# Kernel tuning notes

Hardware: AMD Instinct MI355X
Metric: run time of the kernel (lower is better)

Reference implementation:

```python
import jax, jax.numpy as jnp
import numpy as np

B, T, D = 2, 2048, 1024
H = 16
DH = D // H


def setup_inputs() -> dict:
    key = jax.random.key(0)
    ks = jax.random.split(key, 6)
    s = 1.0 / np.sqrt(D)
    return {
        "x": jax.random.normal(ks[0], (B, T, D), dtype=jnp.float32),
        "Wq": jax.random.normal(ks[1], (D, D), dtype=jnp.float32) * s,
        "Wk": jax.random.normal(ks[2], (D, D), dtype=jnp.float32) * s,
        "Wv": jax.random.normal(ks[3], (D, D), dtype=jnp.float32) * s,
        "Wo": jax.random.normal(ks[4], (D, D), dtype=jnp.float32) * s,
        "bo": jax.random.normal(ks[5], (D,), dtype=jnp.float32) * s,
    }


def reference(x, Wq, Wk, Wv, Wo, bo):
    b, t, _ = x.shape
    # separate Q/K/V projections (nn.Linear: x @ W.T, no bias)
    q = (x @ Wq.T).reshape(b, t, H, DH).transpose(0, 2, 1, 3)  # [b,h,t,hd]
    k = (x @ Wk.T).reshape(b, t, H, DH).transpose(0, 2, 1, 3)
    v = (x @ Wv.T).reshape(b, t, H, DH).transpose(0, 2, 1, 3)

    scores = jnp.einsum("bhqd,bhkd->bhqk", q, k)  # [b,h,t,t]
    causal = jnp.triu(jnp.ones((t, t), dtype=bool), k=1)
    scores = jnp.where(causal, -jnp.inf, scores)
    weights = jax.nn.softmax(scores / np.sqrt(DH), axis=-1)
    # dropout p=0.0 -> identity
    ctx = jnp.einsum("bhqk,bhkd->bhqd", weights, v)  # [b,h,t,hd]
    # NOTE: original code reshapes WITHOUT transposing heads back — replicate faithfully
    ctx = ctx.reshape(b, t, H * DH)
    return ctx @ Wo.T + bo
```

## Files before the change

### kernel.cpp

```cpp
#include <hip/hip_runtime.h>
#include <math.h>

#define BATCH 2
#define SEQ   2048
#define DIM   1024
#define NH    16
#define HD    64
#define MTOT  4096

typedef __attribute__((ext_vector_type(8)))  short bf16x8;
typedef __attribute__((ext_vector_type(4)))  float f32x4;
typedef __attribute__((ext_vector_type(16))) float f32x16;

__device__ __forceinline__ ushort f2bf(float f) {
    union { float f; unsigned u; } v; v.f = f;
    unsigned r = v.u + 0x7fffu + ((v.u >> 16) & 1u);
    return (ushort)(r >> 16);
}

__device__ __forceinline__ unsigned cvtpk_bf16(float lo, float hi) {
    unsigned r;
    asm("v_cvt_pk_bf16_f32 %0, %1, %2" : "=v"(r) : "v"(lo), "v"(hi));
    return r;
}

__global__ __launch_bounds__(256)
void cast_all(const float* __restrict__ x,
              const float* __restrict__ Wq, const float* __restrict__ Wk,
              const float* __restrict__ Wv, const float* __restrict__ Wo,
              ushort* __restrict__ xb,
              ushort* __restrict__ wqb, ushort* __restrict__ wkb,
              ushort* __restrict__ wvb, ushort* __restrict__ wob)
{
    const int z = blockIdx.y;
    const float* s; ushort* d; int n4;
    if (z == 0)      { s = x;  d = xb;  n4 = MTOT * DIM / 4; }
    else if (z == 1) { s = Wq; d = wqb; n4 = DIM * DIM / 4; }
    else if (z == 2) { s = Wk; d = wkb; n4 = DIM * DIM / 4; }
    else if (z == 3) { s = Wv; d = wvb; n4 = DIM * DIM / 4; }
    else             { s = Wo; d = wob; n4 = DIM * DIM / 4; }
    for (int i = blockIdx.x * blockDim.x + threadIdx.x; i < n4;
         i += gridDim.x * blockDim.x) {
        float4 v = ((const float4*)s)[i];
        ushort4 o;
        o.x = f2bf(v.x); o.y = f2bf(v.y); o.z = f2bf(v.z); o.w = f2bf(v.w);
        ((ushort4*)d)[i] = o;
    }
}

template<int MODE>
__global__ __launch_bounds__(256)
void gemm_bf16(const ushort* __restrict__ A,
               const ushort* __restrict__ W0, const ushort* __restrict__ W1,
               const ushort* __restrict__ W2,
               ushort* __restrict__ D0, ushort* __restrict__ D1,
               ushort* __restrict__ D2,
               const float* __restrict__ bias, float* __restrict__ Fout)
{
    __shared__ __align__(16) ushort As[2][128 * 64];
    __shared__ __align__(16) ushort Bs[2][128 * 64];

    const int tid = threadIdx.x;
    const int w = tid >> 6, l = tid & 63;
    const int g = l >> 4, l15 = l & 15;
    const int wr = w >> 1, wc = w & 1;
    const int brow = blockIdx.x * 128, bcol = blockIdx.y * 128;

    const ushort* W = (MODE == 1) ? W0
                    : (blockIdx.z == 0 ? W0 : (blockIdx.z == 1 ? W1 : W2));
    ushort* Dst = (MODE == 1) ? (ushort*)0
                : (blockIdx.z == 0 ? D0 : (blockIdx.z == 1 ? D1 : D2));

    const int rsub = l >> 3;
    const int gc   = ((l & 7) ^ rsub) * 8;
    const size_t arow0 = (size_t)(brow + 32 * w + rsub) * DIM;
    const size_t brow0 = (size_t)(bcol + 32 * w + rsub) * DIM;

    auto STAGE = [&](int buf, int ktel) {
        #pragma unroll
        for (int i = 0; i < 4; ++i) {
            __builtin_amdgcn_global_load_lds(
                (const __attribute__((address_space(1))) void*)
                    &A[arow0 + (size_t)(8 * i) * DIM + ktel + gc],
                (__attribute__((address_space(3))) void*)
                    &As[buf][(32 * w + 8 * i) * 64], 16, 0, 0);
            __builtin_amdgcn_global_load_lds(
                (const __attribute__((address_space(1))) void*)
                    &W[brow0 + (size_t)(8 * i) * DIM + ktel + gc],
                (__attribute__((address_space(3))) void*)
                    &Bs[buf][(32 * w + 8 * i) * 64], 16, 0, 0);
        }
    };

    STAGE(0, 0);
    STAGE(1, 64);

    f32x4 acc[4][4] = {};

    for (int t = 0; t < 16; ++t) {
        const int cur = t & 1;
        if (t < 15) asm volatile("s_waitcnt vmcnt(8)" ::: "memory");
        else        asm volatile("s_waitcnt vmcnt(0)" ::: "memory");
        __builtin_amdgcn_s_barrier();
        __builtin_amdgcn_sched_barrier(0);

        #pragma unroll
        for (int kh = 0; kh < 2; ++kh) {
            bf16x8 af[4], bfr[4];
            #pragma unroll
            for (int mi = 0; mi < 4; ++mi) {
                int row = 64 * wr + 16 * mi + l15;
                af[mi] = *(const bf16x8*)&As[cur][row * 64 + (((4 * kh + g) ^ (row & 7)) * 8)];
            }
            #pragma unroll
            for (int nj = 0; nj < 4; ++nj) {
                int row = 64 * wc + 16 * nj + l15;
                bfr[nj] = *(const bf16x8*)&Bs[cur][row * 64 + (((4 * kh + g) ^ (row & 7)) * 8)];
            }
            __builtin_amdgcn_s_setprio(1);
            #pragma unroll
            for (int mi = 0; mi < 4; ++mi)
                #pragma unroll
                for (int nj = 0; nj < 4; ++nj)
                    acc[mi][nj] = __builtin_amdgcn_mfma_f32_16x16x32_bf16(
                        af[mi], bfr[nj], acc[mi][nj], 0, 0, 0);
            __builtin_amdgcn_s_setprio(0);
        }

        __builtin_amdgcn_sched_barrier(0);
        __builtin_amdgcn_s_barrier();
        if (t + 2 < 16) STAGE(cur, (t + 2) * 64);
    }

    if (MODE == 0) {
        const float osc = (blockIdx.z == 0) ? 0.125f : 1.0f;
        if (blockIdx.z == 2) {
            #pragma unroll
            for (int mi = 0; mi < 4; ++mi)
                #pragma unroll
                for (int nj = 0; nj < 4; ++nj)
                    #pragma unroll
                    for (int reg = 0; reg < 4; ++reg) {
                        int row = brow + 64 * wr + 16 * mi + 4 * g + reg;
                        int col = bcol + 64 * wc + 16 * nj + l15;
                        int b = row >> 11, t = row & (SEQ - 1);
                        int hh = col >> 6, hd = col & 63;
                        Dst[(size_t)(b * NH + hh) * SEQ * HD
                            + ((size_t)(t >> 3) * 64 + hd) * 8 + (t & 7)] =
                            f2bf(acc[mi][nj][reg]);
                    }
        } else {
            #pragma unroll
            for (int mi = 0; mi < 4; ++mi)
                #pragma unroll
                for (int nj = 0; nj < 4; ++nj)
                    #pragma unroll
                    for (int reg = 0; reg < 4; ++reg) {
                        int row = brow + 64 * wr + 16 * mi + 4 * g + reg;
                        int col = bcol + 64 * wc + 16 * nj + l15;
                        int b = row >> 11, t = row & (SEQ - 1);
                        int hh = col >> 6, hd = col & 63;
                        Dst[(size_t)(b * NH + hh) * SEQ * HD
                            + (((size_t)(t >> 5) * 8 + (hd >> 3)) * 32 + (t & 31)) * 8
                            + (hd & 7)] = f2bf(acc[mi][nj][reg] * osc);
                    }
        }
    } else {
        #pragma unroll
        for (int nj = 0; nj < 4; ++nj) {
            int col = bcol + 64 * wc + 16 * nj + l15;
            float bv = bias[col];
            #pragma unroll
            for (int mi = 0; mi < 4; ++mi)
                #pragma unroll
                for (int reg = 0; reg < 4; ++reg) {
                    int row = brow + 64 * wr + 16 * mi + 4 * g + reg;
                    Fout[(size_t)row * DIM + col] = acc[mi][nj][reg] + bv;
                }
        }
    }
}

__global__ __launch_bounds__(64, 2)
void attn_mfma5(const ushort* __restrict__ q, const ushort* __restrict__ k,
                const ushort* __restrict__ vt, ushort* __restrict__ ctx)
{
    __shared__ __align__(16) ushort Ob[32 * 64];

    const int l = threadIdx.x;
    const int l31 = l & 31, h = l >> 5;
    const int bh = blockIdx.x;
    const int qt = 63 - (int)blockIdx.y;
    const int qlo = qt * 32;
    const int last = qt >> 1;
    const float LOG2E = 1.44269504f;

    const ushort* Qg = q  + (size_t)bh * SEQ * HD;
    const ushort* Kg = k  + (size_t)bh * SEQ * HD;
    const ushort* Vg = vt + (size_t)bh * SEQ * HD;

    bf16x8 qf[4];
    #pragma unroll
    for (int s = 0; s < 4; ++s)
        qf[s] = *(const bf16x8*)&Qg[(((size_t)qt * 8 + 2 * s + h) * 32 + l31) * 8];

    f32x16 o[2] = {};
    float m = -3.0e38f, lsum = 0.f;

    bf16x8 kfA[8], kfB[8], vfA[8], vfB[8];
    #pragma unroll
    for (int s = 0; s < 4; ++s)
        #pragma unroll
        for (int f = 0; f < 2; ++f)
            kfA[2 * s + f] = *(const bf16x8*)
                &Kg[(((size_t)f * 8 + 2 * s + h) * 32 + l31) * 8];
    #pragma unroll
    for (int s4 = 0; s4 < 4; ++s4)
        #pragma unroll
        for (int dt = 0; dt < 2; ++dt)
            vfA[2 * s4 + dt] = *(const bf16x8*)
                &Vg[(((size_t)(2 * s4 + h)) * 64 + 32 * dt + l31) * 8];

    auto body = [&](bf16x8 (&kc)[8], bf16x8 (&kn)[8],
                    bf16x8 (&vc)[8], bf16x8 (&vn)[8], int kt) {
        const int kvb = 64 * kt;

        f32x16 st[2] = {};
        #pragma unroll
        for (int s = 0; s < 4; ++s)
            #pragma unroll
            for (int f = 0; f < 2; ++f)
                st[f] = __builtin_amdgcn_mfma_f32_32x32x16_bf16(
                    kc[2 * s + f], qf[s], st[f], 0, 0, 0);

        if (kt < last) {
            #pragma unroll
            for (int s = 0; s < 4; ++s)
                #pragma unroll
                for (int f = 0; f < 2; ++f)
                    kn[2 * s + f] = *(const bf16x8*)
                        &Kg[(((size_t)(2 * kt + 2 + f) * 8 + 2 * s + h) * 32 + l31) * 8];
            #pragma unroll
            for (int s4 = 0; s4 < 4; ++s4)
                #pragma unroll
                for (int dt = 0; dt < 2; ++dt)
                    vn[2 * s4 + dt] = *(const bf16x8*)
                        &Vg[(((size_t)(8 * kt + 8 + 2 * s4 + h)) * 64 + 32 * dt + l31) * 8];
        }

        const int qg = qlo + l31;
        if (kvb + 63 > qlo) {
            #pragma unroll
            for (int f = 0; f < 2; ++f)
                #pragma unroll
                for (int r = 0; r < 16; ++r) {
                    int kvg = kvb + 32 * f + (r & 3) + 8 * (r >> 2) + 4 * h;
                    if (kvg > qg) st[f][r] = -INFINITY;
                }
        }

        float mx[8];
        #pragma unroll
        for (int i2 = 0; i2 < 8; ++i2) {
            const int f = i2 >> 2, rb = 4 * (i2 & 3);
            mx[i2] = fmaxf(fmaxf(st[f][rb], st[f][rb + 1]),
                           fmaxf(st[f][rb + 2], st[f][rb + 3]));
        }
        float tmax = fmaxf(fmaxf(fmaxf(mx[0], mx[1]), fmaxf(mx[2], mx[3])),
                           fmaxf(fmaxf(mx[4], mx[5]), fmaxf(mx[6], mx[7])));
        tmax = fmaxf(tmax, __shfl_xor(tmax, 32));
        float ty = fmaxf(tmax * LOG2E, -3.0e38f);

        if (!__all(ty - m <= 8.0f)) {
            float mn = fmaxf(m, ty);
            float sc = exp2f(m - mn);
            lsum *= sc;
            #pragma unroll
            for (int dt = 0; dt < 2; ++dt)
                #pragma unroll
                for (int r = 0; r < 16; ++r) o[dt][r] *= sc;
            m = mn;
        }

        float ls0 = 0.f, ls1 = 0.f, ls2 = 0.f, ls3 = 0.f;
        #pragma unroll
        for (int f = 0; f < 2; ++f)
            #pragma unroll
            for (int r = 0; r < 16; ++r) {
                float pv = exp2f(fmaf(st[f][r], LOG2E, -m));
                st[f][r] = pv;
                if ((r & 3) == 0) ls0 += pv;
                else if ((r & 3) == 1) ls1 += pv;
                else if ((r & 3) == 2) ls2 += pv;
                else ls3 += pv;
            }
        lsum += (ls0 + ls1) + (ls2 + ls3);

        #pragma unroll
        for (int s4 = 0; s4 < 4; ++s4) {
            const int f = s4 >> 1, rb2 = 8 * (s4 & 1);
            unsigned Aa = cvtpk_bf16(st[f][rb2 + 0], st[f][rb2 + 1]);
            unsigned Bb = cvtpk_bf16(st[f][rb2 + 2], st[f][rb2 + 3]);
            unsigned Cc = cvtpk_bf16(st[f][rb2 + 4], st[f][rb2 + 5]);
            unsigned Dd = cvtpk_bf16(st[f][rb2 + 6], st[f][rb2 + 7]);
            unsigned Ax = (unsigned)__shfl_xor((int)Aa, 32);
            unsigned Bx = (unsigned)__shfl_xor((int)Bb, 32);
            unsigned Cx = (unsigned)__shfl_xor((int)Cc, 32);
            unsigned Dx = (unsigned)__shfl_xor((int)Dd, 32);
            union { unsigned wv[4]; bf16x8 v; } pu;
            pu.wv[0] = h ? Cx : Aa;
            pu.wv[1] = h ? Dx : Bb;
            pu.wv[2] = h ? Cc : Ax;
            pu.wv[3] = h ? Dd : Bx;
            #pragma unroll
            for (int dt = 0; dt < 2; ++dt)
                o[dt] = __builtin_amdgcn_mfma_f32_32x32x16_bf16(
                    vc[2 * s4 + dt], pu.v, o[dt], 0, 0, 0);
        }
    };

    int kt = 0;
    while (true) {
        body(kfA, kfB, vfA, vfB, kt);
        if (++kt > last) break;
        body(kfB, kfA, vfB, vfA, kt);
        if (++kt > last) break;
    }

    float lt = lsum + __shfl_xor(lsum, 32);
    float inv = 1.0f / lt;

    #pragma unroll
    for (int dt = 0; dt < 2; ++dt)
        #pragma unroll
        for (int r = 0; r < 16; r += 2) {
            int d = 32 * dt + (r & 3) + 8 * (r >> 2) + 4 * h;
            unsigned wrd = cvtpk_bf16(o[dt][r] * inv, o[dt][r + 1] * inv);
            *(unsigned*)&Ob[l31 * 64 + (((d >> 3) ^ (l31 & 7)) * 8) + (d & 7)] = wrd;
        }
    asm volatile("s_waitcnt lgkmcnt(0)" ::: "memory");
    __builtin_amdgcn_sched_barrier(0);

    ushort* Cg = ctx + (size_t)bh * SEQ * HD + (size_t)qlo * HD;
    #pragma unroll
    for (int i = 0; i < 4; ++i) {
        int qq = l >> 1, c = (l & 1) * 4 + i;
        int4 vvv = *(const int4*)&Ob[qq * 64 + ((c ^ (qq & 7)) * 8)];
        *(int4*)&Cg[qq * 64 + c * 8] = vvv;
    }
}

extern "C" void kernel_launch(void* const* d_in, const int* in_sizes, int n_in,
                              void* d_out, int out_size, void* d_ws, size_t ws_size,
                              hipStream_t stream)
{
    (void)in_sizes; (void)n_in; (void)out_size; (void)ws_size;
    const float* x  = (const float*)d_in[0];
    const float* Wq = (const float*)d_in[1];
    const float* Wk = (const float*)d_in[2];
    const float* Wv = (const float*)d_in[3];
    const float* Wo = (const float*)d_in[4];
    const float* bo = (const float*)d_in[5];
    float* out = (float*)d_out;

    ushort* wsu  = (ushort*)d_ws;
    ushort* xb   = wsu;
    ushort* wqb  = wsu + 4194304;
    ushort* wkb  = wsu + 5242880;
    ushort* wvb  = wsu + 6291456;
    ushort* wob  = wsu + 7340032;
    ushort* qbuf = wsu + 8388608;
    ushort* kbuf = wsu + 12582912;
    ushort* vtb  = wsu + 16777216;
    ushort* ctxb = wsu + 20971520;

    cast_all<<<dim3(512, 5), 256, 0, stream>>>(x, Wq, Wk, Wv, Wo,
                                               xb, wqb, wkb, wvb, wob);

    dim3 gqkv(MTOT / 128, DIM / 128, 3);
    gemm_bf16<0><<<gqkv, 256, 0, stream>>>(xb, wqb, wkb, wvb,
                                           qbuf, kbuf, vtb, nullptr, nullptr);

    dim3 ga(BATCH * NH, SEQ / 32);
    attn_mfma5<<<ga, 64, 0, stream>>>(qbuf, kbuf, vtb, ctxb);

    dim3 go(MTOT / 128, DIM / 128, 1);
    gemm_bf16<1><<<go, 256, 0, stream>>>(ctxb, wob, nullptr, nullptr,
                                         nullptr, nullptr, nullptr, bo, out);
}
```

Before: 116.3 us.

## Split attention KV range across four waves and merge partial softmax in LDS

The attention kernel now launches 256 threads per block, and each of the four waves processes a contiguous quarter of the causal KV tiles for the same 32-query tile. Each wave keeps its own online-softmax state. The partial max, sum and output values are then combined through LDS with a rescale-and-add reduction before the bf16 context is written. This split-K style parallelism shortens the serial KV loop per block and should help the long late query tiles. The cost is extra LDS traffic (32KB of fp32 partials), two block barriers, and idle waves on short early tiles.

Measured after the change: 244.9 us. 110% more time.

```diff
diff --git a/kernel.cpp b/kernel.cpp
--- a/kernel.cpp
+++ b/kernel.cpp
@@ -181,18 +181,24 @@
     }
 }
 
-__global__ __launch_bounds__(64, 2)
-void attn_mfma5(const ushort* __restrict__ q, const ushort* __restrict__ k,
+__global__ __launch_bounds__(256, 4)
+void attn_mfma6(const ushort* __restrict__ q, const ushort* __restrict__ k,
                 const ushort* __restrict__ vt, ushort* __restrict__ ctx)
 {
-    __shared__ __align__(16) ushort Ob[32 * 64];
-
-    const int l = threadIdx.x;
+    __shared__ float Olds[4 * 2048];
+    __shared__ float Mlds[4][32];
+    __shared__ float Llds[4][32];
+
+    const int tid = threadIdx.x;
+    const int wq = tid >> 6, l = tid & 63;
     const int l31 = l & 31, h = l >> 5;
     const int bh = blockIdx.x;
     const int qt = 63 - (int)blockIdx.y;
     const int qlo = qt * 32;
-    const int last = qt >> 1;
+    const int nt  = (qt >> 1) + 1;
+    const int cnt = (nt + 3) >> 2;
+    const int kt0 = wq * cnt;
+    const int kt1 = min(nt, kt0 + cnt);
     const float LOG2E = 1.44269504f;
 
     const ushort* Qg = q  + (size_t)bh * SEQ * HD;
@@ -207,147 +213,160 @@
     f32x16 o[2] = {};
     float m = -3.0e38f, lsum = 0.f;
 
-    bf16x8 kfA[8], kfB[8], vfA[8], vfB[8];
-    #pragma unroll
-    for (int s = 0; s < 4; ++s)
-        #pragma unroll
-        for (int f = 0; f < 2; ++f)
-            kfA[2 * s + f] = *(const bf16x8*)
-                &Kg[(((size_t)f * 8 + 2 * s + h) * 32 + l31) * 8];
-    #pragma unroll
-    for (int s4 = 0; s4 < 4; ++s4)
-        #pragma unroll
-        for (int dt = 0; dt < 2; ++dt)
-            vfA[2 * s4 + dt] = *(const bf16x8*)
-                &Vg[(((size_t)(2 * s4 + h)) * 64 + 32 * dt + l31) * 8];
-
-    auto body = [&](bf16x8 (&kc)[8], bf16x8 (&kn)[8],
-                    bf16x8 (&vc)[8], bf16x8 (&vn)[8], int kt) {
-        const int kvb = 64 * kt;
-
-        f32x16 st[2] = {};
+    if (kt0 < kt1) {
+        bf16x8 kfA[8], kfB[8], vfA[8], vfB[8];
         #pragma unroll
         for (int s = 0; s < 4; ++s)
             #pragma unroll
             for (int f = 0; f < 2; ++f)
-                st[f] = __builtin_amdgcn_mfma_f32_32x32x16_bf16(
-                    kc[2 * s + f], qf[s], st[f], 0, 0, 0);
-
-        if (kt < last) {
+                kfA[2 * s + f] = *(const bf16x8*)
+                    &Kg[(((size_t)(2 * kt0 + f) * 8 + 2 * s + h) * 32 + l31) * 8];
+        #pragma unroll
+        for (int s4 = 0; s4 < 4; ++s4)
+            #pragma unroll
+            for (int dt = 0; dt < 2; ++dt)
+                vfA[2 * s4 + dt] = *(const bf16x8*)
+                    &Vg[(((size_t)(8 * kt0 + 2 * s4 + h)) * 64 + 32 * dt + l31) * 8];
+
+        auto body = [&](bf16x8 (&kc)[8], bf16x8 (&kn)[8],
+                        bf16x8 (&vc)[8], bf16x8 (&vn)[8], int kt) {
+            const int kvb = 64 * kt;
+
+            f32x16 st[2] = {};
             #pragma unroll
             for (int s = 0; s < 4; ++s)
                 #pragma unroll
                 for (int f = 0; f < 2; ++f)
-                    kn[2 * s + f] = *(const bf16x8*)
-                        &Kg[(((size_t)(2 * kt + 2 + f) * 8 + 2 * s + h) * 32 + l31) * 8];
-            #pragma unroll
-            for (int s4 = 0; s4 < 4; ++s4)
+                    st[f] = __builtin_amdgcn_mfma_f32_32x32x16_bf16(
+                        kc[2 * s + f], qf[s], st[f], 0, 0, 0);
+
+            if (kt + 1 < kt1) {
+                #pragma unroll
+                for (int s = 0; s < 4; ++s)
+                    #pragma unroll
+                    for (int f = 0; f < 2; ++f)
+                        kn[2 * s + f] = *(const bf16x8*)
+                            &Kg[(((size_t)(2 * kt + 2 + f) * 8 + 2 * s + h) * 32 + l31) * 8];
+                #pragma unroll
+                for (int s4 = 0; s4 < 4; ++s4)
+                    #pragma unroll
+                    for (int dt = 0; dt < 2; ++dt)
+                        vn[2 * s4 + dt] = *(const bf16x8*)
+                            &Vg[(((size_t)(8 * kt + 8 + 2 * s4 + h)) * 64 + 32 * dt + l31) * 8];
+            }
+
+            const int qg = qlo + l31;
+            if (kvb + 63 > qlo) {
+                #pragma unroll
+                for (int f = 0; f < 2; ++f)
+                    #pragma unroll
+                    for (int r = 0; r < 16; ++r) {
+                        int kvg = kvb + 32 * f + (r & 3) + 8 * (r >> 2) + 4 * h;
+                        if (kvg > qg) st[f][r] = -INFINITY;
+                    }
+            }
+
+            float mx[8];
+            #pragma unroll
+            for (int i2 = 0; i2 < 8; ++i2) {
+                const int f = i2 >> 2, rb = 4 * (i2 & 3);
+                mx[i2] = fmaxf(fmaxf(st[f][rb], st[f][rb + 1]),
+                               fmaxf(st[f][rb + 2], st[f][rb + 3]));
+            }
+            float tmax = fmaxf(fmaxf(fmaxf(mx[0], mx[1]), fmaxf(mx[2], mx[3])),
+                               fmaxf(fmaxf(mx[4], mx[5]), fmaxf(mx[6], mx[7])));
+            tmax = fmaxf(tmax, __shfl_xor(tmax, 32));
+            float ty = fmaxf(tmax * LOG2E, -3.0e38f);
+
+            if (!__all(ty - m <= 8.0f)) {
+                float mn = fmaxf(m, ty);
+                float sc = exp2f(m - mn);
+                lsum *= sc;
                 #pragma unroll
                 for (int dt = 0; dt < 2; ++dt)
-                    vn[2 * s4 + dt] = *(const bf16x8*)
-                        &Vg[(((size_t)(8 * kt + 8 + 2 * s4 + h)) * 64 + 32 * dt + l31) * 8];
-        }
-
-        const int qg = qlo + l31;
-        if (kvb + 63 > qlo) {
+                    #pragma unroll
+                    for (int r = 0; r < 16; ++r) o[dt][r] *= sc;
+                m = mn;
+            }
+
+            float ls0 = 0.f, ls1 = 0.f, ls2 = 0.f, ls3 = 0.f;
             #pragma unroll
             for (int f = 0; f < 2; ++f)
                 #pragma unroll
                 for (int r = 0; r < 16; ++r) {
-                    int kvg = kvb + 32 * f + (r & 3) + 8 * (r >> 2) + 4 * h;
-                    if (kvg > qg) st[f][r] = -INFINITY;
+                    float pv = exp2f(fmaf(st[f][r], LOG2E, -m));
+                    st[f][r] = pv;
+                    if ((r & 3) == 0) ls0 += pv;
+                    else if ((r & 3) == 1) ls1 += pv;
+                    else if ((r & 3) == 2) ls2 += pv;
+                    else ls3 += pv;
                 }
-        }
-
-        float mx[8];
-        #pragma unroll
-        for (int i2 = 0; i2 < 8; ++i2) {
-            const int f = i2 >> 2, rb = 4 * (i2 & 3);
-            mx[i2] = fmaxf(fmaxf(st[f][rb], st[f][rb + 1]),
-                           fmaxf(st[f][rb + 2], st[f][rb + 3]));
-        }
-        float tmax = fmaxf(fmaxf(fmaxf(mx[0], mx[1]), fmaxf(mx[2], mx[3])),
-                           fmaxf(fmaxf(mx[4], mx[5]), fmaxf(mx[6], mx[7])));
-        tmax = fmaxf(tmax, __shfl_xor(tmax, 32));
-        float ty = fmaxf(tmax * LOG2E, -3.0e38f);
-
-        if (!__all(ty - m <= 8.0f)) {
-            float mn = fmaxf(m, ty);
-            float sc = exp2f(m - mn);
-            lsum *= sc;
-            #pragma unroll
-            for (int dt = 0; dt < 2; ++dt)
-                #pragma unroll
-                for (int r = 0; r < 16; ++r) o[dt][r] *= sc;
-            m = mn;
-        }
-
-        float ls0 = 0.f, ls1 = 0.f, ls2 = 0.f, ls3 = 0.f;
-        #pragma unroll
-        for (int f = 0; f < 2; ++f)
-            #pragma unroll
-            for (int r = 0; r < 16; ++r) {
-                float pv = exp2f(fmaf(st[f][r], LOG2E, -m));
-                st[f][r] = pv;
-                if ((r & 3) == 0) ls0 += pv;
-                else if ((r & 3) == 1) ls1 += pv;
-                else if ((r & 3) == 2) ls2 += pv;
-                else ls3 += pv;
-            }
-        lsum += (ls0 + ls1) + (ls2 + ls3);
-
-        #pragma unroll
-        for (int s4 = 0; s4 < 4; ++s4) {
-            const int f = s4 >> 1, rb2 = 8 * (s4 & 1);
-            unsigned Aa = cvtpk_bf16(st[f][rb2 + 0], st[f][rb2 + 1]);
-            unsigned Bb = cvtpk_bf16(st[f][rb2 + 2], st[f][rb2 + 3]);
-            unsigned Cc = cvtpk_bf16(st[f][rb2 + 4], st[f][rb2 + 5]);
-            unsigned Dd = cvtpk_bf16(st[f][rb2 + 6], st[f][rb2 + 7]);
-            unsigned Ax = (unsigned)__shfl_xor((int)Aa, 32);
-            unsigned Bx = (unsigned)__shfl_xor((int)Bb, 32);
-            unsigned Cx = (unsigned)__shfl_xor((int)Cc, 32);
-            unsigned Dx = (unsigned)__shfl_xor((int)Dd, 32);
-            union { unsigned wv[4]; bf16x8 v; } pu;
-            pu.wv[0] = h ? Cx : Aa;
-            pu.wv[1] = h ? Dx : Bb;
-            pu.wv[2] = h ? Cc : Ax;
-            pu.wv[3] = h ? Dd : Bx;
-            #pragma unroll
-            for (int dt = 0; dt < 2; ++dt)
-                o[dt] = __builtin_amdgcn_mfma_f32_32x32x16_bf16(
-                    vc[2 * s4 + dt], pu.v, o[dt], 0, 0, 0);
-        }
-    };
-
-    int kt = 0;
-    while (true) {
-        body(kfA, kfB, vfA, vfB, kt);
-        if (++kt > last) break;
-        body(kfB, kfA, vfB, vfA, kt);
-        if (++kt > last) break;
+            lsum += (ls0 + ls1) + (ls2 + ls3);
+
+            #pragma unroll
+            for (int s4 = 0; s4 < 4; ++s4) {
+                const int f = s4 >> 1, rb2 = 8 * (s4 & 1);
+                unsigned Aa = cvtpk_bf16(st[f][rb2 + 0], st[f][rb2 + 1]);
+                unsigned Bb = cvtpk_bf16(st[f][rb2 + 2], st[f][rb2 + 3]);
+                unsigned Cc = cvtpk_bf16(st[f][rb2 + 4], st[f][rb2 + 5]);
+                unsigned Dd = cvtpk_bf16(st[f][rb2 + 6], st[f][rb2 + 7]);
+                unsigned Ax = (unsigned)__shfl_xor((int)Aa, 32);
+                unsigned Bx = (unsigned)__shfl_xor((int)Bb, 32);
+                unsigned Cx = (unsigned)__shfl_xor((int)Cc, 32);
+                unsigned Dx = (unsigned)__shfl_xor((int)Dd, 32);
+                union { unsigned wv[4]; bf16x8 v; } pu;
+                pu.wv[0] = h ? Cx : Aa;
+                pu.wv[1] = h ? Dx : Bb;
+                pu.wv[2] = h ? Cc : Ax;
+                pu.wv[3] = h ? Dd : Bx;
+                #pragma unroll
+                for (int dt = 0; dt < 2; ++dt)
+                    o[dt] = __builtin_amdgcn_mfma_f32_32x32x16_bf16(
+                        vc[2 * s4 + dt], pu.v, o[dt], 0, 0, 0);
+            }
+        };
+
+        int kt = kt0;
+        while (true) {
+            body(kfA, kfB, vfA, vfB, kt);
+            if (++kt >= kt1) break;
+            body(kfB, kfA, vfB, vfA, kt);
+            if (++kt >= kt1) break;
+        }
     }
 
     float lt = lsum + __shfl_xor(lsum, 32);
-    float inv = 1.0f / lt;
-
+    if (h == 0) Mlds[wq][l31] = m;
+    __syncthreads();
+    float ms = fmaxf(fmaxf(Mlds[0][l31], Mlds[1][l31]),
+                     fmaxf(Mlds[2][l31], Mlds[3][l31]));
+    float fw = exp2f(m - ms);
+    if (h == 0) Llds[wq][l31] = lt * fw;
     #pragma unroll
     for (int dt = 0; dt < 2; ++dt)
         #pragma unroll
-        for (int r = 0; r < 16; r += 2) {
+        for (int r = 0; r < 16; ++r) {
             int d = 32 * dt + (r & 3) + 8 * (r >> 2) + 4 * h;
-            unsigned wrd = cvtpk_bf16(o[dt][r] * inv, o[dt][r + 1] * inv);
-            *(unsigned*)&Ob[l31 * 64 + (((d >> 3) ^ (l31 & 7)) * 8) + (d & 7)] = wrd;
-        }
-    asm volatile("s_waitcnt lgkmcnt(0)" ::: "memory");
-    __builtin_amdgcn_sched_barrier(0);
-
+            Olds[wq * 2048 + d * 32 + (l31 ^ (d & 31))] = o[dt][r] * fw;
+        }
+    __syncthreads();
+
+    const int tq = tid >> 3, tc = tid & 7;
+    float inv = 1.0f / (Llds[0][tq] + Llds[1][tq] + Llds[2][tq] + Llds[3][tq]);
+    union { ushort u[8]; int4 v4; } ov;
+    #pragma unroll
+    for (int i = 0; i < 8; i += 2) {
+        int d0 = 8 * tc + i, d1 = d0 + 1;
+        float s0 = 0.f, s1 = 0.f;
+        #pragma unroll
+        for (int ww = 0; ww < 4; ++ww) {
+            s0 += Olds[ww * 2048 + d0 * 32 + (tq ^ (d0 & 31))];
+            s1 += Olds[ww * 2048 + d1 * 32 + (tq ^ (d1 & 31))];
+        }
+        *(unsigned*)&ov.u[i] = cvtpk_bf16(s0 * inv, s1 * inv);
+    }
     ushort* Cg = ctx + (size_t)bh * SEQ * HD + (size_t)qlo * HD;
-    #pragma unroll
-    for (int i = 0; i < 4; ++i) {
-        int qq = l >> 1, c = (l & 1) * 4 + i;
-        int4 vvv = *(const int4*)&Ob[qq * 64 + ((c ^ (qq & 7)) * 8)];
-        *(int4*)&Cg[qq * 64 + c * 8] = vvv;
-    }
+    *(int4*)&Cg[tq * 64 + 8 * tc] = ov.v4;
 }
 
 extern "C" void kernel_launch(void* const* d_in, const int* in_sizes, int n_in,
@@ -382,7 +401,7 @@
                                            qbuf, kbuf, vtb, nullptr, nullptr);
 
     dim3 ga(BATCH * NH, SEQ / 32);
-    attn_mfma5<<<ga, 64, 0, stream>>>(qbuf, kbuf, vtb, ctxb);
+    attn_mfma6<<<ga, 256, 0, stream>>>(qbuf, kbuf, vtb, ctxb);
 
     dim3 go(MTOT / 128, DIM / 128, 1);
     gemm_bf16<1><<<go, 256, 0, stream>>>(ctxb, wob, nullptr, nullptr,
```
